# Kernel tuning notes

Measured on AMD Instinct MI355X. Metric: run time of the kernel, lower is better.

The kernel has to match this reference:

```python
import jax, jax.numpy as jnp
import numpy as np

D = 256   # vec_dim
H = 8     # head_num
P = 1024  # patch_num
N = 8     # batch


def setup_inputs() -> dict:
    key = jax.random.key(0)
    ks = jax.random.split(key, 11)
    s = 0.05
    return {
        "inputs": jax.random.normal(ks[0], (N, D, P), dtype=jnp.float32),
        "pos_mat": jax.random.normal(ks[1], (1, H, P, P), dtype=jnp.float32),
        "Wk": jax.random.normal(ks[2], (H * D, D), dtype=jnp.float32) * s,
        "bk": jax.random.normal(ks[3], (H * D,), dtype=jnp.float32) * s,
        "Wq": jax.random.normal(ks[4], (H * D, D), dtype=jnp.float32) * s,
        "bq": jax.random.normal(ks[5], (H * D,), dtype=jnp.float32) * s,
        "Wv": jax.random.normal(ks[6], (H * D, D), dtype=jnp.float32) * s,
        "bv": jax.random.normal(ks[7], (H * D,), dtype=jnp.float32) * s,
        "Wo": jax.random.normal(ks[8], (D, H * D), dtype=jnp.float32) * s,
        "bo": jax.random.normal(ks[9], (D,), dtype=jnp.float32) * s,
    }


def reference(inputs, pos_mat, Wk, bk, Wq, bq, Wv, bv, Wo, bo):
    n, d, p = inputs.shape  # [N, D, P]
    h = Wk.shape[0] // d
    # 1x1 Conv1d == per-position GEMM: [H*D,D] x [N,D,P] -> [N,H*D,P] -> [N,H,D,P]
    k = (jnp.einsum('od,ndp->nop', Wk, inputs) + bk[:, None]).reshape(n, h, d, p)
    q = (jnp.einsum('od,ndp->nop', Wq, inputs) + bq[:, None]).reshape(n, h, d, p)
    v = (jnp.einsum('od,ndp->nop', Wv, inputs) + bv[:, None]).reshape(n, h, d, p)
    # attn[n,h,kpos,qpos] = K^T Q / sqrt(D), shape [N,H,P,P]
    attn = jnp.einsum('nhdk,nhdq->nhkq', k, q) / jnp.sqrt(jnp.asarray(d, inputs.dtype))
    attn = attn + pos_mat
    # NOTE: original uses Softmax(dim=2), i.e. over the KEY axis, not the last dim
    w = jax.nn.softmax(attn, axis=2)
    out = jnp.einsum('nhdk,nhkq->nhdq', v, w).reshape(n, h * d, p)
    return jnp.einsum('oi,nip->nop', Wo, out) + bo[:, None]
```

## Files before the change

### kernel.cpp

```cpp
#include <hip/hip_runtime.h>

typedef __bf16 bf16;
typedef __attribute__((ext_vector_type(8))) __bf16 bf16x8;
typedef __attribute__((ext_vector_type(4))) __bf16 bf16x4;
typedef __attribute__((ext_vector_type(2))) __bf16 bf16x2;
typedef __attribute__((ext_vector_type(4))) float f32x4;

#define MFMA16(a, b, c) __builtin_amdgcn_mfma_f32_16x16x32_bf16(a, b, c, 0, 0, 0)

__device__ __forceinline__ void gload_lds16(const void* g, void* l) {
  __builtin_amdgcn_global_load_lds(
      (const __attribute__((address_space(1))) void*)g,
      (__attribute__((address_space(3))) void*)l, 16, 0, 0);
}

constexpr int NH = 8, DD = 256, PP = 1024;

constexpr size_t WB_YT  = 33554432;
constexpr size_t WB_XB  = 67108864;
constexpr size_t WB_XBT = 71303168;
constexpr size_t WB_MB  = 75497472;
constexpr size_t WB_UB  = 76546048;
constexpr size_t WB_U   = 77594624;
constexpr size_t WB_BP  = 77602816;

constexpr int FL_PT0  = 0;
constexpr int FL_XT0  = 16384;
constexpr int FL_LRED = 0;
constexpr int FL_SZ   = 81920;

#define EXP_SHIFT 4.0f

__global__ __launch_bounds__(256, 1) void msa_mu(
    const float* __restrict__ Wk, const float* __restrict__ Wq,
    const float* __restrict__ Wo, const float* __restrict__ Wv,
    bf16* __restrict__ Mb, bf16* __restrict__ Ub) {
  __shared__ float lds[64 * 65];
  const int t = threadIdx.x;
  const int i0 = (blockIdx.x >> 2) * 64;
  const int jq = blockIdx.x & 3;
  const int h = blockIdx.y;
  const int mode = blockIdx.z;
  const int j0 = (t & 31) * 2 + jq * 64;
  const int i8 = t >> 5;
  float acc0[8], acc1[8];
#pragma unroll
  for (int r = 0; r < 8; ++r) { acc0[r] = 0.f; acc1[r] = 0.f; }
  const float* __restrict__ W2 = (mode == 0) ? Wq : Wv;
  for (int dhc = 0; dhc < 256; dhc += 64) {
    __syncthreads();
    if (mode == 0) {
#pragma unroll
      for (int s = 0; s < 16; ++s) {
        int f = t + s * 256;
        int dh = f >> 6, ii = f & 63;
        lds[dh * 65 + ii] = Wk[(h * 256 + dhc + dh) * 256 + i0 + ii];
      }
    } else {
#pragma unroll
      for (int s = 0; s < 16; ++s) {
        int f = t + s * 256;
        int oo = f >> 6, dh = f & 63;
        lds[dh * 65 + oo] = Wo[(i0 + oo) * 2048 + h * 256 + dhc + dh];
      }
    }
    __syncthreads();
    for (int dl = 0; dl < 64; ++dl) {
      float2 wv = *reinterpret_cast<const float2*>(&W2[(h * 256 + dhc + dl) * 256 + j0]);
#pragma unroll
      for (int r = 0; r < 8; ++r) {
        float x = lds[dl * 65 + i8 * 8 + r];
        acc0[r] = fmaf(x, wv.x, acc0[r]);
        acc1[r] = fmaf(x, wv.y, acc1[r]);
      }
    }
  }
  if (mode == 0) {
#pragma unroll
    for (int r = 0; r < 8; ++r) {
      int i = i0 + i8 * 8 + r;
      bf16x2 v = { (__bf16)(acc0[r] * 0.0625f), (__bf16)(acc1[r] * 0.0625f) };
      *reinterpret_cast<bf16x2*>(&Mb[h * 65536 + i * 256 + j0]) = v;
    }
  } else {
#pragma unroll
    for (int r = 0; r < 8; ++r) {
      int o = i0 + i8 * 8 + r;
      bf16x2 v = { (__bf16)acc0[r], (__bf16)acc1[r] };
      *reinterpret_cast<bf16x2*>(&Ub[o * 2048 + h * 256 + j0]) = v;
    }
  }
}

__global__ void msa_u(const float* __restrict__ Wk, const float* __restrict__ bq,
                      float* __restrict__ u) {
  __shared__ float bqs[256];
  const int h = blockIdx.x, t = threadIdx.x;
  bqs[t] = bq[h * 256 + t];
  __syncthreads();
  float acc = 0.f;
  for (int dh = 0; dh < 256; ++dh)
    acc = fmaf(Wk[(h * 256 + dh) * 256 + t], bqs[dh], acc);
  u[h * 256 + t] = acc * 0.0625f;
}

__global__ void msa_bp(const float* __restrict__ Wo, const float* __restrict__ bv,
                       const float* __restrict__ bo, float* __restrict__ bp) {
  const int o = blockIdx.x, t = threadIdx.x;
  float acc = 0.f;
  for (int f = t; f < 2048; f += 256)
    acc = fmaf(Wo[o * 2048 + f], bv[f], acc);
#pragma unroll
  for (int m = 32; m >= 1; m >>= 1) acc += __shfl_down(acc, m);
  __shared__ float part[4];
  if ((t & 63) == 0) part[t >> 6] = acc;
  __syncthreads();
  if (t == 0) bp[o] = bo[o] + part[0] + part[1] + part[2] + part[3];
}

__global__ __launch_bounds__(256, 4) void msa_cvtX(
    const float* __restrict__ X, bf16* __restrict__ Xb, bf16* __restrict__ XbT) {
  __shared__ __bf16 tl[64 * 68];
  const int t = threadIdx.x;
  const int p0 = blockIdx.x * 64, d0 = blockIdx.y * 64, n = blockIdx.z;
  const float* __restrict__ Xn = X + (size_t)n * DD * PP;
#pragma unroll
  for (int rr = 0; rr < 4; ++rr) {
    int r = (t >> 4) + rr * 16, c = (t & 15) * 4;
    float4 v = *reinterpret_cast<const float4*>(Xn + (size_t)(d0 + r) * PP + p0 + c);
    bf16x4 pk = { (__bf16)v.x, (__bf16)v.y, (__bf16)v.z, (__bf16)v.w };
    *reinterpret_cast<bf16x4*>(Xb + (size_t)n * DD * PP + (size_t)(d0 + r) * PP + p0 + c) = pk;
    *reinterpret_cast<bf16x4*>(&tl[r * 68 + c]) = pk;
  }
  __syncthreads();
#pragma unroll
  for (int rr = 0; rr < 4; ++rr) {
    int pr = (t >> 4) + rr * 16, dc = (t & 15) * 4;
    bf16x4 pk = { tl[(dc + 0) * 68 + pr], tl[(dc + 1) * 68 + pr],
                  tl[(dc + 2) * 68 + pr], tl[(dc + 3) * 68 + pr] };
    *reinterpret_cast<bf16x4*>(XbT + (size_t)n * PP * DD + (size_t)(p0 + pr) * DD + d0 + dc) = pk;
  }
}

__global__ __launch_bounds__(256, 2) void msa_flash(
    const bf16* __restrict__ XbT, const bf16* __restrict__ Xb,
    const bf16* __restrict__ Mb, const float* __restrict__ u,
    const float* __restrict__ pos, bf16* __restrict__ Yt) {
  extern __shared__ char smc[];
  const int t = threadIdx.x;
  const int lane = t & 63, w = t >> 6;
  const int g = lane >> 4, ln = lane & 15;
  const int kw = w >> 1, qw = w & 1;
  const int bid = blockIdx.x;
  const int h = bid & 7, qt = (bid >> 3) & 15, n = bid >> 7;
  const int qg0 = qt * 64, nh = n * 8 + h;
  const bf16* __restrict__ XbTn = XbT + (size_t)n * (PP * DD);
  const bf16* __restrict__ Xbn  = Xb + (size_t)n * (DD * PP);
  const bf16* __restrict__ Mh   = Mb + (size_t)h * (DD * DD);
  const float* __restrict__ posh = pos + (size_t)h * (PP * PP);
  float* lredp = (float*)(smc + FL_LRED);

  const int grl = lane >> 5;
  const int gcb = lane & 31;

  {
    bf16x8 ta[4][8];
#pragma unroll
    for (int mq = 0; mq < 4; ++mq)
#pragma unroll
      for (int s = 0; s < 8; ++s)
        ta[mq][s] = *reinterpret_cast<const bf16x8*>(
            XbTn + (size_t)(qg0 + mq * 16 + ln) * DD + s * 32 + g * 8);
#pragma unroll
    for (int ni = 0; ni < 4; ++ni) {
      const int i_ = w * 64 + ni * 16 + ln;
      bf16x8 tb8[8];
#pragma unroll
      for (int s = 0; s < 8; ++s)
        tb8[s] = *reinterpret_cast<const bf16x8*>(Mh + (size_t)i_ * DD + s * 32 + g * 8);
      const float uv = u[h * 256 + i_];
#pragma unroll
      for (int mq = 0; mq < 4; ++mq) {
        f32x4 acc = {0.f, 0.f, 0.f, 0.f};
#pragma unroll
        for (int s = 0; s < 8; ++s) acc = MFMA16(ta[mq][s], tb8[s], acc);
#pragma unroll
        for (int r = 0; r < 4; ++r) {
          const int q = mq * 16 + 4 * g + r;
          const int addr = FL_XT0 + q * 512 +
              (((w * 8 + ni * 2 + (ln >> 3)) ^ (q & 7)) << 4) + (ln & 7) * 2;
          *reinterpret_cast<__bf16*>(smc + addr) = (__bf16)(acc[r] + uv);
        }
      }
    }
  }
  __syncthreads();

  bf16x8 tb[2][8];
#pragma unroll
  for (int nq = 0; nq < 2; ++nq) {
    const int q_ = qw * 32 + nq * 16 + ln;
#pragma unroll
    for (int s = 0; s < 8; ++s)
      tb[nq][s] = *reinterpret_cast<const bf16x8*>(
          smc + FL_XT0 + q_ * 512 + (((4 * s + g) ^ (q_ & 7)) << 4));
  }
  __syncthreads();

#pragma unroll
  for (int c = 0; c < 8; ++c) {
    const int row = w * 16 + c * 2 + grl;
    const int cbg = gcb ^ (row & 7);
    gload_lds16(XbTn + (size_t)row * DD + cbg * 8,
                smc + FL_XT0 + w * 8192 + c * 1024);
  }
  float posv[2][2][4];
#pragma unroll
  for (int mt = 0; mt < 2; ++mt)
#pragma unroll
    for (int nq = 0; nq < 2; ++nq) {
      const float* pr = posh + (size_t)(kw * 32 + mt * 16 + 4 * g) * PP +
                        qg0 + qw * 32 + nq * 16 + ln;
#pragma unroll
      for (int r = 0; r < 4; ++r) posv[mt][nq][r] = pr[(size_t)r * PP];
    }
  __syncthreads();

  float lsum[2] = {0.f, 0.f};
  f32x4 yacc[4][4];
#pragma unroll
  for (int a = 0; a < 4; ++a)
#pragma unroll
    for (int b = 0; b < 4; ++b) { f32x4 z = {0.f, 0.f, 0.f, 0.f}; yacc[a][b] = z; }

  for (int kt = 0; kt < 16; ++kt) {
    const int kg0 = kt * 64;
    const int curXT = FL_XT0 + (kt & 1) * 32768;
    const int nxtXT = FL_XT0 + ((kt + 1) & 1) * 32768;
    const int curPT = FL_PT0 + (kt & 1) * 8192;
    if (kt < 15) {
#pragma unroll
      for (int c = 0; c < 8; ++c) {
        const int row = w * 16 + c * 2 + grl;
        const int cbg = gcb ^ (row & 7);
        gload_lds16(XbTn + (size_t)(kg0 + 64 + row) * DD + cbg * 8,
                    smc + nxtXT + w * 8192 + c * 1024);
      }
    }
    bf16x8 xv[2][4];
#pragma unroll
    for (int ks = 0; ks < 2; ++ks)
#pragma unroll
      for (int nd = 0; nd < 4; ++nd)
        xv[ks][nd] = *reinterpret_cast<const bf16x8*>(
            Xbn + (size_t)(w * 64 + nd * 16 + ln) * PP + kg0 + ks * 32 + g * 8);
    f32x4 sacc[2][2];
#pragma unroll
    for (int a = 0; a < 2; ++a)
#pragma unroll
      for (int b = 0; b < 2; ++b) { f32x4 z = {0.f, 0.f, 0.f, 0.f}; sacc[a][b] = z; }
    __builtin_amdgcn_s_setprio(1);
#pragma unroll
    for (int mt = 0; mt < 2; ++mt) {
      const int row = kw * 32 + mt * 16 + ln;
      bf16x8 af8[8];
#pragma unroll
      for (int s = 0; s < 8; ++s)
        af8[s] = *reinterpret_cast<const bf16x8*>(
            smc + curXT + row * 512 + (((4 * s + g) ^ (row & 7)) << 4));
#pragma unroll
      for (int s = 0; s < 8; ++s)
#pragma unroll
        for (int nq = 0; nq < 2; ++nq)
          sacc[mt][nq] = MFMA16(af8[s], tb[nq][s], sacc[mt][nq]);
    }
    __builtin_amdgcn_s_setprio(0);
    float posvn[2][2][4];
    if (kt < 15) {
#pragma unroll
      for (int mt = 0; mt < 2; ++mt)
#pragma unroll
        for (int nq = 0; nq < 2; ++nq) {
          const float* pr = posh + (size_t)(kg0 + 64 + kw * 32 + mt * 16 + 4 * g) * PP +
                            qg0 + qw * 32 + nq * 16 + ln;
#pragma unroll
          for (int r = 0; r < 4; ++r) posvn[mt][nq][r] = pr[(size_t)r * PP];
        }
    }
#pragma unroll
    for (int mt = 0; mt < 2; ++mt)
#pragma unroll
      for (int nq = 0; nq < 2; ++nq) {
        bf16x4 pk;
#pragma unroll
        for (int r = 0; r < 4; ++r) {
          float e = __expf(sacc[mt][nq][r] + posv[mt][nq][r] - EXP_SHIFT);
          lsum[nq] += e;
          pk[r] = (__bf16)e;
        }
        const int q_ = qw * 32 + nq * 16 + ln;
        *reinterpret_cast<bf16x4*>(smc + curPT + q_ * 128 +
            (((kw * 4 + mt * 2 + (g >> 1)) ^ (q_ & 7)) << 4) + ((g & 1) << 3)) = pk;
      }
    __syncthreads();
    __builtin_amdgcn_s_setprio(1);
#pragma unroll
    for (int ks = 0; ks < 2; ++ks) {
      bf16x8 pa[4];
#pragma unroll
      for (int mq = 0; mq < 4; ++mq) {
        const int q_ = mq * 16 + ln;
        pa[mq] = *reinterpret_cast<const bf16x8*>(
            smc + curPT + q_ * 128 + (((4 * ks + g) ^ (q_ & 7)) << 4));
      }
#pragma unroll
      for (int mq = 0; mq < 4; ++mq)
#pragma unroll
        for (int nd = 0; nd < 4; ++nd)
          yacc[mq][nd] = MFMA16(pa[mq], xv[ks][nd], yacc[mq][nd]);
    }
    __builtin_amdgcn_s_setprio(0);
    if (kt < 15) {
#pragma unroll
      for (int mt = 0; mt < 2; ++mt)
#pragma unroll
        for (int nq = 0; nq < 2; ++nq)
#pragma unroll
          for (int r = 0; r < 4; ++r) posv[mt][nq][r] = posvn[mt][nq][r];
    }
  }

#pragma unroll
  for (int nq = 0; nq < 2; ++nq) {
    lsum[nq] += __shfl_xor(lsum[nq], 16);
    lsum[nq] += __shfl_xor(lsum[nq], 32);
  }
  if (lane < 16) {
#pragma unroll
    for (int nq = 0; nq < 2; ++nq)
      lredp[kw * 64 + qw * 32 + nq * 16 + ln] = lsum[nq];
  }
  __syncthreads();
  bf16* __restrict__ Ytp = Yt + (size_t)nh * (PP * DD);
#pragma unroll
  for (int mq = 0; mq < 4; ++mq) {
    f32x4 l0 = *reinterpret_cast<const f32x4*>(lredp + mq * 16 + 4 * g);
    f32x4 l1 = *reinterpret_cast<const f32x4*>(lredp + 64 + mq * 16 + 4 * g);
    f32x4 inv;
#pragma unroll
    for (int r = 0; r < 4; ++r) inv[r] = 1.0f / (l0[r] + l1[r]);
#pragma unroll
    for (int nd = 0; nd < 4; ++nd)
#pragma unroll
      for (int r = 0; r < 4; ++r)
        Ytp[(size_t)(qg0 + mq * 16 + 4 * g + r) * DD + w * 64 + nd * 16 + ln] =
            (__bf16)(yacc[mq][nd][r] * inv[r]);
  }
}

__global__ __launch_bounds__(256, 3) void msa_final4(
    const bf16* __restrict__ Ub, const bf16* __restrict__ Yt,
    const float* __restrict__ bp, float* __restrict__ out) {
  __shared__ char lsd[49152];
  const int t = threadIdx.x, lane = t & 63, w = t >> 6;
  const int g = lane >> 4, ln = lane & 15;
  const int pw = w & 1, ow = w >> 1;
  const int pb = blockIdx.x * 128, ob = blockIdx.y * 64, n = blockIdx.z;
  const bf16* __restrict__ Ytn = Yt + (size_t)n * 8 * (PP * DD);
  f32x4 acc[2][4];
#pragma unroll
  for (int a = 0; a < 2; ++a)
#pragma unroll
    for (int b = 0; b < 4; ++b) { f32x4 z = {0.f, 0.f, 0.f, 0.f}; acc[a][b] = z; }

  uint4 areg[2], breg[4];
  {
#pragma unroll
    for (int j = 0; j < 2; ++j) {
      int u_ = t + j * 256;
      areg[j] = *reinterpret_cast<const uint4*>(
          Ub + (size_t)(ob + (u_ >> 3)) * 2048 + 0 + (u_ & 7) * 8);
    }
#pragma unroll
    for (int j = 0; j < 4; ++j) {
      int v_ = t + j * 256;
      breg[j] = *reinterpret_cast<const uint4*>(
          Ytn + ((size_t)0 * PP + pb + (v_ >> 3)) * DD + 0 + (v_ & 7) * 8);
    }
#pragma unroll
    for (int j = 0; j < 2; ++j) {
      int u_ = t + j * 256, row = u_ >> 3, cb = u_ & 7;
      *reinterpret_cast<uint4*>(lsd + row * 128 + ((cb ^ (row & 7)) << 4)) = areg[j];
    }
#pragma unroll
    for (int j = 0; j < 4; ++j) {
      int v_ = t + j * 256, row = v_ >> 3, cb = v_ & 7;
      *reinterpret_cast<uint4*>(lsd + 8192 + row * 128 + ((cb ^ (row & 7)) << 4)) = breg[j];
    }
  }
  __syncthreads();

  for (int kc = 0; kc < 32; ++kc) {
    const int cur = (kc & 1) * 24576;
    const int nxt = ((kc + 1) & 1) * 24576;
    if (kc < 31) {
      const int k1 = (kc + 1) * 64, hh = k1 >> 8, dd = k1 & 255;
#pragma unroll
      for (int j = 0; j < 2; ++j) {
        int u_ = t + j * 256;
        areg[j] = *reinterpret_cast<const uint4*>(
            Ub + (size_t)(ob + (u_ >> 3)) * 2048 + k1 + (u_ & 7) * 8);
      }
#pragma unroll
      for (int j = 0; j < 4; ++j) {
        int v_ = t + j * 256;
        breg[j] = *reinterpret_cast<const uint4*>(
            Ytn + ((size_t)hh * PP + pb + (v_ >> 3)) * DD + dd + (v_ & 7) * 8);
      }
    }
#pragma unroll
    for (int ks = 0; ks < 2; ++ks) {
      bf16x8 a[2], b[4];
#pragma unroll
      for (int mo = 0; mo < 2; ++mo) {
        const int row = ow * 32 + mo * 16 + ln;
        a[mo] = *reinterpret_cast<const bf16x8*>(
            lsd + cur + row * 128 + (((4 * ks + g) ^ (row & 7)) << 4));
      }
#pragma unroll
      for (int np = 0; np < 4; ++np) {
        const int row = pw * 64 + np * 16 + ln;
        b[np] = *reinterpret_cast<const bf16x8*>(
            lsd + cur + 8192 + row * 128 + (((4 * ks + g) ^ (row & 7)) << 4));
      }
#pragma unroll
      for (int mo = 0; mo < 2; ++mo)
#pragma unroll
        for (int np = 0; np < 4; ++np) acc[mo][np] = MFMA16(a[mo], b[np], acc[mo][np]);
    }
    if (kc < 31) {
#pragma unroll
      for (int j = 0; j < 2; ++j) {
        int u_ = t + j * 256, row = u_ >> 3, cb = u_ & 7;
        *reinterpret_cast<uint4*>(lsd + nxt + row * 128 + ((cb ^ (row & 7)) << 4)) = areg[j];
      }
#pragma unroll
      for (int j = 0; j < 4; ++j) {
        int v_ = t + j * 256, row = v_ >> 3, cb = v_ & 7;
        *reinterpret_cast<uint4*>(lsd + nxt + 8192 + row * 128 + ((cb ^ (row & 7)) << 4)) = breg[j];
      }
    }
    __syncthreads();
  }

#pragma unroll
  for (int mo = 0; mo < 2; ++mo) {
    f32x4 bv = *reinterpret_cast<const f32x4*>(bp + ob + ow * 32 + mo * 16 + 4 * g);
#pragma unroll
    for (int np = 0; np < 4; ++np)
#pragma unroll
      for (int r = 0; r < 4; ++r) {
        const int o = ob + ow * 32 + mo * 16 + 4 * g + r;
        out[((size_t)n * DD + o) * PP + pb + pw * 64 + np * 16 + ln] =
            acc[mo][np][r] + bv[r];
      }
  }
}

extern "C" void kernel_launch(void* const* d_in, const int* in_sizes, int n_in,
                              void* d_out, int out_size, void* d_ws, size_t ws_size,
                              hipStream_t stream) {
  const float* X   = (const float*)d_in[0];
  const float* pos = (const float*)d_in[1];
  const float* Wk  = (const float*)d_in[2];
  const float* Wq  = (const float*)d_in[4];
  const float* bq  = (const float*)d_in[5];
  const float* Wv  = (const float*)d_in[6];
  const float* bv  = (const float*)d_in[7];
  const float* Wo  = (const float*)d_in[8];
  const float* bo  = (const float*)d_in[9];

  char* ws = (char*)d_ws;
  bf16* Yt  = (bf16*)(ws + WB_YT);
  bf16* Xb  = (bf16*)(ws + WB_XB);
  bf16* XbT = (bf16*)(ws + WB_XBT);
  bf16* Mb  = (bf16*)(ws + WB_MB);
  bf16* Ub  = (bf16*)(ws + WB_UB);
  float* u  = (float*)(ws + WB_U);
  float* bp = (float*)(ws + WB_BP);
  float* out = (float*)d_out;

  hipFuncSetAttribute(reinterpret_cast<const void*>(msa_flash),
                      hipFuncAttributeMaxDynamicSharedMemorySize, FL_SZ);

  msa_cvtX<<<dim3(16, 4, 8), 256, 0, stream>>>(X, Xb, XbT);
  msa_mu<<<dim3(16, 8, 2), 256, 0, stream>>>(Wk, Wq, Wo, Wv, Mb, Ub);
  msa_u<<<8, 256, 0, stream>>>(Wk, bq, u);
  msa_bp<<<256, 256, 0, stream>>>(Wo, bv, bo, bp);
  msa_flash<<<1024, 256, FL_SZ, stream>>>(XbT, Xb, Mb, u, pos, Yt);
  msa_final4<<<dim3(8, 4, 8), 256, 0, stream>>>(Ub, Yt, bp, out);
}
```

Before: 286.5 us.

## Widen flash tile to 128 queries with 8 waves and bf16 pos matrix

Adds a pre-pass that converts the fp32 positional matrix to bf16 in workspace, and the flash kernel then reads bf16 pos values inside each key tile instead of prefetching fp32 values one tile ahead. The flash kernel now uses 512-thread blocks, each covering 128 queries, so every staged K tile is reused across twice as many queries and the grid shrinks to 512 blocks. It also reorders block indices so batch varies fastest and drops the s_setprio hints. In exchange it adds a full pass over the 32MB pos tensor, larger LDS use, one block per CU, and a possible stall from the loss of pos prefetching.

New measurement: 310.2 us. +8.3%, slower.

```diff
diff --git a/kernel.cpp b/kernel.cpp
--- a/kernel.cpp
+++ b/kernel.cpp
@@ -16,6 +16,7 @@
 
 constexpr int NH = 8, DD = 256, PP = 1024;
 
+constexpr size_t WB_POSB = 0;
 constexpr size_t WB_YT  = 33554432;
 constexpr size_t WB_XB  = 67108864;
 constexpr size_t WB_XBT = 71303168;
@@ -25,11 +26,21 @@
 constexpr size_t WB_BP  = 77602816;
 
 constexpr int FL_PT0  = 0;
-constexpr int FL_XT0  = 16384;
+constexpr int FL_XT0  = 32768;
 constexpr int FL_LRED = 0;
-constexpr int FL_SZ   = 81920;
+constexpr int FL_SZ   = 98304;
 
 #define EXP_SHIFT 4.0f
+
+__global__ __launch_bounds__(256, 4) void msa_cvtPos(
+    const float* __restrict__ pos, bf16* __restrict__ posb) {
+  const size_t i = ((size_t)blockIdx.x * 256 + threadIdx.x) * 8;
+  float4 a = *reinterpret_cast<const float4*>(pos + i);
+  float4 b = *reinterpret_cast<const float4*>(pos + i + 4);
+  bf16x8 pk = { (__bf16)a.x, (__bf16)a.y, (__bf16)a.z, (__bf16)a.w,
+                (__bf16)b.x, (__bf16)b.y, (__bf16)b.z, (__bf16)b.w };
+  *reinterpret_cast<bf16x8*>(posb + i) = pk;
+}
 
 __global__ __launch_bounds__(256, 1) void msa_mu(
     const float* __restrict__ Wk, const float* __restrict__ Wq,
@@ -142,53 +153,51 @@
   }
 }
 
-__global__ __launch_bounds__(256, 2) void msa_flash(
+__global__ __launch_bounds__(512, 1) void msa_flash(
     const bf16* __restrict__ XbT, const bf16* __restrict__ Xb,
     const bf16* __restrict__ Mb, const float* __restrict__ u,
-    const float* __restrict__ pos, bf16* __restrict__ Yt) {
+    const bf16* __restrict__ posb, bf16* __restrict__ Yt) {
   extern __shared__ char smc[];
   const int t = threadIdx.x;
   const int lane = t & 63, w = t >> 6;
   const int g = lane >> 4, ln = lane & 15;
-  const int kw = w >> 1, qw = w & 1;
+  const int kw = w >> 2, qs = w & 3;
   const int bid = blockIdx.x;
-  const int h = bid & 7, qt = (bid >> 3) & 15, n = bid >> 7;
-  const int qg0 = qt * 64, nh = n * 8 + h;
+  const int n = bid & 7, qt = (bid >> 3) & 7, h = bid >> 6;
+  const int qg0 = qt * 128, nh = n * 8 + h;
   const bf16* __restrict__ XbTn = XbT + (size_t)n * (PP * DD);
   const bf16* __restrict__ Xbn  = Xb + (size_t)n * (DD * PP);
   const bf16* __restrict__ Mh   = Mb + (size_t)h * (DD * DD);
-  const float* __restrict__ posh = pos + (size_t)h * (PP * PP);
+  const bf16* __restrict__ posh = posb + (size_t)h * (PP * PP);
   float* lredp = (float*)(smc + FL_LRED);
 
   const int grl = lane >> 5;
   const int gcb = lane & 31;
 
   {
-    bf16x8 ta[4][8];
-#pragma unroll
-    for (int mq = 0; mq < 4; ++mq)
-#pragma unroll
-      for (int s = 0; s < 8; ++s)
-        ta[mq][s] = *reinterpret_cast<const bf16x8*>(
-            XbTn + (size_t)(qg0 + mq * 16 + ln) * DD + s * 32 + g * 8);
-#pragma unroll
-    for (int ni = 0; ni < 4; ++ni) {
-      const int i_ = w * 64 + ni * 16 + ln;
+#pragma unroll
+    for (int ni = 0; ni < 2; ++ni) {
+      const int i_ = w * 32 + ni * 16 + ln;
       bf16x8 tb8[8];
 #pragma unroll
       for (int s = 0; s < 8; ++s)
         tb8[s] = *reinterpret_cast<const bf16x8*>(Mh + (size_t)i_ * DD + s * 32 + g * 8);
       const float uv = u[h * 256 + i_];
 #pragma unroll
-      for (int mq = 0; mq < 4; ++mq) {
+      for (int mq = 0; mq < 8; ++mq) {
+        bf16x8 ta[8];
+#pragma unroll
+        for (int s = 0; s < 8; ++s)
+          ta[s] = *reinterpret_cast<const bf16x8*>(
+              XbTn + (size_t)(qg0 + mq * 16 + ln) * DD + s * 32 + g * 8);
         f32x4 acc = {0.f, 0.f, 0.f, 0.f};
 #pragma unroll
-        for (int s = 0; s < 8; ++s) acc = MFMA16(ta[mq][s], tb8[s], acc);
+        for (int s = 0; s < 8; ++s) acc = MFMA16(ta[s], tb8[s], acc);
 #pragma unroll
         for (int r = 0; r < 4; ++r) {
           const int q = mq * 16 + 4 * g + r;
-          const int addr = FL_XT0 + q * 512 +
-              (((w * 8 + ni * 2 + (ln >> 3)) ^ (q & 7)) << 4) + (ln & 7) * 2;
+          const int blk = w * 4 + ni * 2 + (ln >> 3);
+          const int addr = FL_XT0 + q * 512 + ((blk ^ (q & 7)) << 4) + (ln & 7) * 2;
           *reinterpret_cast<__bf16*>(smc + addr) = (__bf16)(acc[r] + uv);
         }
       }
@@ -199,7 +208,7 @@
   bf16x8 tb[2][8];
 #pragma unroll
   for (int nq = 0; nq < 2; ++nq) {
-    const int q_ = qw * 32 + nq * 16 + ln;
+    const int q_ = qs * 32 + nq * 16 + ln;
 #pragma unroll
     for (int s = 0; s < 8; ++s)
       tb[nq][s] = *reinterpret_cast<const bf16x8*>(
@@ -208,58 +217,57 @@
   __syncthreads();
 
 #pragma unroll
-  for (int c = 0; c < 8; ++c) {
-    const int row = w * 16 + c * 2 + grl;
+  for (int c = 0; c < 4; ++c) {
+    const int row = w * 8 + c * 2 + grl;
     const int cbg = gcb ^ (row & 7);
     gload_lds16(XbTn + (size_t)row * DD + cbg * 8,
-                smc + FL_XT0 + w * 8192 + c * 1024);
-  }
-  float posv[2][2][4];
-#pragma unroll
-  for (int mt = 0; mt < 2; ++mt)
-#pragma unroll
-    for (int nq = 0; nq < 2; ++nq) {
-      const float* pr = posh + (size_t)(kw * 32 + mt * 16 + 4 * g) * PP +
-                        qg0 + qw * 32 + nq * 16 + ln;
-#pragma unroll
-      for (int r = 0; r < 4; ++r) posv[mt][nq][r] = pr[(size_t)r * PP];
-    }
+                smc + FL_XT0 + w * 4096 + c * 1024);
+  }
   __syncthreads();
 
   float lsum[2] = {0.f, 0.f};
-  f32x4 yacc[4][4];
-#pragma unroll
-  for (int a = 0; a < 4; ++a)
-#pragma unroll
-    for (int b = 0; b < 4; ++b) { f32x4 z = {0.f, 0.f, 0.f, 0.f}; yacc[a][b] = z; }
+  f32x4 yacc[8][2];
+#pragma unroll
+  for (int a = 0; a < 8; ++a)
+#pragma unroll
+    for (int b = 0; b < 2; ++b) { f32x4 z = {0.f, 0.f, 0.f, 0.f}; yacc[a][b] = z; }
 
   for (int kt = 0; kt < 16; ++kt) {
     const int kg0 = kt * 64;
     const int curXT = FL_XT0 + (kt & 1) * 32768;
     const int nxtXT = FL_XT0 + ((kt + 1) & 1) * 32768;
-    const int curPT = FL_PT0 + (kt & 1) * 8192;
+    const int curPT = FL_PT0 + (kt & 1) * 16384;
     if (kt < 15) {
 #pragma unroll
-      for (int c = 0; c < 8; ++c) {
-        const int row = w * 16 + c * 2 + grl;
+      for (int c = 0; c < 4; ++c) {
+        const int row = w * 8 + c * 2 + grl;
         const int cbg = gcb ^ (row & 7);
         gload_lds16(XbTn + (size_t)(kg0 + 64 + row) * DD + cbg * 8,
-                    smc + nxtXT + w * 8192 + c * 1024);
-      }
-    }
-    bf16x8 xv[2][4];
+                    smc + nxtXT + w * 4096 + c * 1024);
+      }
+    }
+    bf16x8 xv[2][2];
 #pragma unroll
     for (int ks = 0; ks < 2; ++ks)
 #pragma unroll
-      for (int nd = 0; nd < 4; ++nd)
+      for (int nd = 0; nd < 2; ++nd)
         xv[ks][nd] = *reinterpret_cast<const bf16x8*>(
-            Xbn + (size_t)(w * 64 + nd * 16 + ln) * PP + kg0 + ks * 32 + g * 8);
+            Xbn + (size_t)(w * 32 + nd * 16 + ln) * PP + kg0 + ks * 32 + g * 8);
+    float posv[2][2][4];
+#pragma unroll
+    for (int mt = 0; mt < 2; ++mt)
+#pragma unroll
+      for (int nq = 0; nq < 2; ++nq) {
+        const bf16* pr = posh + (size_t)(kg0 + kw * 32 + mt * 16 + 4 * g) * PP +
+                         qg0 + qs * 32 + nq * 16 + ln;
+#pragma unroll
+        for (int r = 0; r < 4; ++r) posv[mt][nq][r] = (float)pr[(size_t)r * PP];
+      }
     f32x4 sacc[2][2];
 #pragma unroll
     for (int a = 0; a < 2; ++a)
 #pragma unroll
       for (int b = 0; b < 2; ++b) { f32x4 z = {0.f, 0.f, 0.f, 0.f}; sacc[a][b] = z; }
-    __builtin_amdgcn_s_setprio(1);
 #pragma unroll
     for (int mt = 0; mt < 2; ++mt) {
       const int row = kw * 32 + mt * 16 + ln;
@@ -273,19 +281,6 @@
 #pragma unroll
         for (int nq = 0; nq < 2; ++nq)
           sacc[mt][nq] = MFMA16(af8[s], tb[nq][s], sacc[mt][nq]);
-    }
-    __builtin_amdgcn_s_setprio(0);
-    float posvn[2][2][4];
-    if (kt < 15) {
-#pragma unroll
-      for (int mt = 0; mt < 2; ++mt)
-#pragma unroll
-        for (int nq = 0; nq < 2; ++nq) {
-          const float* pr = posh + (size_t)(kg0 + 64 + kw * 32 + mt * 16 + 4 * g) * PP +
-                            qg0 + qw * 32 + nq * 16 + ln;
-#pragma unroll
-          for (int r = 0; r < 4; ++r) posvn[mt][nq][r] = pr[(size_t)r * PP];
-        }
     }
 #pragma unroll
     for (int mt = 0; mt < 2; ++mt)
@@ -298,35 +293,25 @@
           lsum[nq] += e;
           pk[r] = (__bf16)e;
         }
-        const int q_ = qw * 32 + nq * 16 + ln;
+        const int q_ = qs * 32 + nq * 16 + ln;
         *reinterpret_cast<bf16x4*>(smc + curPT + q_ * 128 +
             (((kw * 4 + mt * 2 + (g >> 1)) ^ (q_ & 7)) << 4) + ((g & 1) << 3)) = pk;
       }
     __syncthreads();
-    __builtin_amdgcn_s_setprio(1);
 #pragma unroll
     for (int ks = 0; ks < 2; ++ks) {
-      bf16x8 pa[4];
-#pragma unroll
-      for (int mq = 0; mq < 4; ++mq) {
+      bf16x8 pa[8];
+#pragma unroll
+      for (int mq = 0; mq < 8; ++mq) {
         const int q_ = mq * 16 + ln;
         pa[mq] = *reinterpret_cast<const bf16x8*>(
             smc + curPT + q_ * 128 + (((4 * ks + g) ^ (q_ & 7)) << 4));
       }
 #pragma unroll
-      for (int mq = 0; mq < 4; ++mq)
-#pragma unroll
-        for (int nd = 0; nd < 4; ++nd)
+      for (int mq = 0; mq < 8; ++mq)
+#pragma unroll
+        for (int nd = 0; nd < 2; ++nd)
           yacc[mq][nd] = MFMA16(pa[mq], xv[ks][nd], yacc[mq][nd]);
-    }
-    __builtin_amdgcn_s_setprio(0);
-    if (kt < 15) {
-#pragma unroll
-      for (int mt = 0; mt < 2; ++mt)
-#pragma unroll
-        for (int nq = 0; nq < 2; ++nq)
-#pragma unroll
-          for (int r = 0; r < 4; ++r) posv[mt][nq][r] = posvn[mt][nq][r];
     }
   }
 
@@ -338,22 +323,22 @@
   if (lane < 16) {
 #pragma unroll
     for (int nq = 0; nq < 2; ++nq)
-      lredp[kw * 64 + qw * 32 + nq * 16 + ln] = lsum[nq];
+      lredp[kw * 128 + qs * 32 + nq * 16 + ln] = lsum[nq];
   }
   __syncthreads();
   bf16* __restrict__ Ytp = Yt + (size_t)nh * (PP * DD);
 #pragma unroll
-  for (int mq = 0; mq < 4; ++mq) {
+  for (int mq = 0; mq < 8; ++mq) {
     f32x4 l0 = *reinterpret_cast<const f32x4*>(lredp + mq * 16 + 4 * g);
-    f32x4 l1 = *reinterpret_cast<const f32x4*>(lredp + 64 + mq * 16 + 4 * g);
+    f32x4 l1 = *reinterpret_cast<const f32x4*>(lredp + 128 + mq * 16 + 4 * g);
     f32x4 inv;
 #pragma unroll
     for (int r = 0; r < 4; ++r) inv[r] = 1.0f / (l0[r] + l1[r]);
 #pragma unroll
-    for (int nd = 0; nd < 4; ++nd)
+    for (int nd = 0; nd < 2; ++nd)
 #pragma unroll
       for (int r = 0; r < 4; ++r)
-        Ytp[(size_t)(qg0 + mq * 16 + 4 * g + r) * DD + w * 64 + nd * 16 + ln] =
+        Ytp[(size_t)(qg0 + mq * 16 + 4 * g + r) * DD + w * 32 + nd * 16 + ln] =
             (__bf16)(yacc[mq][nd][r] * inv[r]);
   }
 }
@@ -481,6 +466,7 @@
   const float* bo  = (const float*)d_in[9];
 
   char* ws = (char*)d_ws;
+  bf16* posb = (bf16*)(ws + WB_POSB);
   bf16* Yt  = (bf16*)(ws + WB_YT);
   bf16* Xb  = (bf16*)(ws + WB_XB);
   bf16* XbT = (bf16*)(ws + WB_XBT);
@@ -493,10 +479,11 @@
   hipFuncSetAttribute(reinterpret_cast<const void*>(msa_flash),
                       hipFuncAttributeMaxDynamicSharedMemorySize, FL_SZ);
 
+  msa_cvtPos<<<4096, 256, 0, stream>>>(pos, posb);
   msa_cvtX<<<dim3(16, 4, 8), 256, 0, stream>>>(X, Xb, XbT);
   msa_mu<<<dim3(16, 8, 2), 256, 0, stream>>>(Wk, Wq, Wo, Wv, Mb, Ub);
   msa_u<<<8, 256, 0, stream>>>(Wk, bq, u);
   msa_bp<<<256, 256, 0, stream>>>(Wo, bv, bo, bp);
-  msa_flash<<<1024, 256, FL_SZ, stream>>>(XbT, Xb, Mb, u, pos, Yt);
+  msa_flash<<<512, 512, FL_SZ, stream>>>(XbT, Xb, Mb, u, posb, Yt);
   msa_final4<<<dim3(8, 4, 8), 256, 0, stream>>>(Ub, Yt, bp, out);
 }
```
